# Kernel tuning notes

Hardware: AMD Instinct MI355X
Metric: run time of the kernel (lower is better)

## Reference

```python
import jax, jax.numpy as jnp
import numpy as np

V, H, L, NH, I, P, B, S = 30000, 768, 12, 12, 3072, 512, 8, 512
D = H // NH  # 64, size_per_head
STD = 0.02
LN_EPS = 1e-3  # Keras LayerNormalization default epsilon


def setup_inputs() -> dict:
    key = jax.random.key(0)
    ks = jax.random.split(key, 16)
    n = lambda k, shape: (jax.random.normal(k, shape, jnp.float32) * STD)
    return {
        "input_ids": jax.random.randint(ks[0], (B, S), 0, V, dtype=jnp.int32),
        "input_mask": jnp.ones((B, S), jnp.int32),
        "token_type_ids": jnp.zeros((B, S), jnp.int32),
        "tok_emb": n(ks[1], (V, H)),
        "pos_emb": n(ks[2], (P, H)),
        "type_emb": n(ks[3], (2, H)),
        "emb_ln_g": jnp.ones((H,), jnp.float32),
        "emb_ln_b": jnp.zeros((H,), jnp.float32),
        "Wq": n(ks[4], (L, H, H)), "bq": jnp.zeros((L, H), jnp.float32),
        "Wk": n(ks[5], (L, H, H)), "bk": jnp.zeros((L, H), jnp.float32),
        "Wv": n(ks[6], (L, H, H)), "bv": jnp.zeros((L, H), jnp.float32),
        "Wo": n(ks[7], (L, H, H)), "bo": jnp.zeros((L, H), jnp.float32),
        "ln1_g": jnp.ones((L, H), jnp.float32), "ln1_b": jnp.zeros((L, H), jnp.float32),
        "Wi": n(ks[8], (L, H, I)), "bi": jnp.zeros((L, I), jnp.float32),
        "Wd": n(ks[9], (L, I, H)), "bd": jnp.zeros((L, H), jnp.float32),
        "ln2_g": jnp.ones((L, H), jnp.float32), "ln2_b": jnp.zeros((L, H), jnp.float32),
    }


def layer_norm(x, g, b):
    mu = jnp.mean(x, axis=-1, keepdims=True)
    var = jnp.mean(jnp.square(x - mu), axis=-1, keepdims=True)
    return (x - mu) * jax.lax.rsqrt(var + LN_EPS) * g + b


def bert_forward(input_ids, input_mask, token_type_ids,
                 tok_emb, pos_emb, type_emb, emb_ln_g, emb_ln_b,
                 Wq, bq, Wk, bk, Wv, bv, Wo, bo, ln1_g, ln1_b,
                 Wi, bi, Wd, bd, ln2_g, ln2_b):
    b, s = input_ids.shape
    # embeddings: token + segment + position, then layernorm (dropout off at inference)
    x = tok_emb[input_ids] + type_emb[token_type_ids] + pos_emb[:s][None, :, :]
    x = layer_norm(x, emb_ln_g, emb_ln_b)

    # additive attention bias from 2D mask: (1 - m) * -10000, broadcast over heads/queries
    mask_bias = (1.0 - input_mask.astype(jnp.float32))[:, None, None, :] * -10000.0  # [b,1,1,s]
    scale = 1.0 / np.sqrt(float(D))

    def block(h, p):
        wq, bq_, wk, bk_, wv, bv_, wo, bo_, g1, b1, wi, bi_, wd, bd_, g2, b2 = p
        # QKV projections, split heads -> [b, nh, s, d]
        split = lambda t: t.reshape(b, s, NH, D).transpose(0, 2, 1, 3)
        q = split(h @ wq + bq_)
        k = split(h @ wk + bk_)
        v = split(h @ wv + bv_)
        scores = jnp.einsum('bhqd,bhkd->bhqk', q, k) * scale + mask_bias
        probs = jax.nn.softmax(scores, axis=-1)
        o = jnp.einsum('bhqk,bhkd->bhqd', probs, v)
        o = o.transpose(0, 2, 1, 3).reshape(b, s, H)
        attn = layer_norm(o @ wo + bo_ + h, g1, b1)
        ffn = jax.nn.gelu(attn @ wi + bi_, approximate=False) @ wd + bd_
        out = layer_norm(ffn + attn, g2, b2)
        return out, None

    params = (Wq, bq, Wk, bk, Wv, bv, Wo, bo, ln1_g, ln1_b, Wi, bi, Wd, bd, ln2_g, ln2_b)
    x, _ = jax.lax.scan(block, x, params)
    return x


def reference(input_ids, input_mask, token_type_ids,
              tok_emb, pos_emb, type_emb, emb_ln_g, emb_ln_b,
              Wq, bq, Wk, bk, Wv, bv, Wo, bo, ln1_g, ln1_b,
              Wi, bi, Wd, bd, ln2_g, ln2_b):
    return bert_forward(input_ids, input_mask, token_type_ids,
                        tok_emb, pos_emb, type_emb, emb_ln_g, emb_ln_b,
                        Wq, bq, Wk, bk, Wv, bv, Wo, bo, ln1_g, ln1_b,
                        Wi, bi, Wd, bd, ln2_g, ln2_b)
```

## Files before the change

### kernel.cpp

```cpp
#include <hip/hip_runtime.h>
#include <math.h>

#define NHEADS 12
#define DHEAD  64
#define SEQL   512
#define HID    768
#define IMID   3072
#define NTOK   4096
#define NLAY   12
#define QKVW   2304

typedef __attribute__((ext_vector_type(8))) short short8;
typedef __attribute__((ext_vector_type(4))) float f32x4;

__device__ __forceinline__ short f2b(float f) {
    union { float f; unsigned u; } v; v.f = f;
    unsigned r = (v.u + 0x7fffu + ((v.u >> 16) & 1u)) >> 16;
    return (short)r;
}
__device__ __forceinline__ float b2f(short h) {
    union { unsigned u; float f; } v; v.u = ((unsigned)(unsigned short)h) << 16;
    return v.f;
}
__device__ __forceinline__ void mfma16(f32x4& c, short8 a, short8 b) {
    asm volatile("v_mfma_f32_16x16x32_bf16 %0, %1, %2, %0" : "+v"(c) : "v"(a), "v"(b));
}
__device__ __forceinline__ void accfence() {
    __builtin_amdgcn_sched_barrier(0);
    asm volatile("s_nop 7\ns_nop 7\ns_nop 7\ns_nop 7");
    __builtin_amdgcn_sched_barrier(0);
}
__device__ __forceinline__ void gload_lds16(const void* g, void* l) {
    __builtin_amdgcn_global_load_lds(
        (const __attribute__((address_space(1))) unsigned int*)g,
        (__attribute__((address_space(3))) unsigned int*)l, 16, 0, 0);
}
__device__ __forceinline__ float gelu_f(float v) {
    float x = v * 0.70710678118f;
    float ax = fabsf(x);
    float t = 1.0f / (1.0f + 0.3275911f * ax);
    float p = ((((1.061405429f * t - 1.453152027f) * t) + 1.421413741f) * t
               - 0.284496736f) * t + 0.254829592f;
    float e = p * t * __expf(-x * x);
    float er = 1.0f - e;
    er = x < 0.f ? -er : er;
    return 0.5f * v * (1.0f + er);
}

__global__ __launch_bounds__(256) void wconv_k(
    const float* __restrict__ src, short* __restrict__ dst,
    int K, int N, size_t dlsz, int rowStart, float scale)
{
    __shared__ short t[64][72];
    src += (size_t)blockIdx.z * K * N;
    dst += (size_t)blockIdx.z * dlsz;
    const int k0 = blockIdx.x * 64, n0 = blockIdx.y * 64;
    const int kr = threadIdx.x >> 2, q = threadIdx.x & 3;
    const float* s = src + (size_t)(k0 + kr) * N + n0 + q * 16;
#pragma unroll
    for (int j = 0; j < 16; j += 4) {
        float4 v = *reinterpret_cast<const float4*>(s + j);
        t[q * 16 + j + 0][kr] = f2b(v.x * scale);
        t[q * 16 + j + 1][kr] = f2b(v.y * scale);
        t[q * 16 + j + 2][kr] = f2b(v.z * scale);
        t[q * 16 + j + 3][kr] = f2b(v.w * scale);
    }
    __syncthreads();
    const int r = threadIdx.x >> 2;
    short* d = dst + (size_t)(rowStart + n0 + r) * K + k0 + q * 16;
    *reinterpret_cast<short8*>(d)     = *reinterpret_cast<short8*>(&t[r][q * 16]);
    *reinterpret_cast<short8*>(d + 8) = *reinterpret_cast<short8*>(&t[r][q * 16 + 8]);
}

__global__ __launch_bounds__(256) void bpack_k(
    const float* __restrict__ bq, const float* __restrict__ bk,
    const float* __restrict__ bv, float* __restrict__ dst)
{
    int i = blockIdx.x * 256 + threadIdx.x;
    if (i >= NLAY * QKVW) return;
    int l = i / QKVW, c = i % QKVW;
    float v = c < 768 ? 0.125f * bq[l * 768 + c]
            : c < 1536 ? bk[l * 768 + c - 768] : bv[l * 768 + c - 1536];
    dst[i] = v;
}

__global__ __launch_bounds__(256) void embed_ln_k(
    const int* __restrict__ ids, const int* __restrict__ tti,
    const float* __restrict__ tokE, const float* __restrict__ posE,
    const float* __restrict__ typE, const float* __restrict__ g,
    const float* __restrict__ bb, float* __restrict__ x, short* __restrict__ xb)
{
    __shared__ float red[8];
    const int t = blockIdx.x, s = t & (SEQL - 1);
    const int id = ids[t], ty = tti[t];
    float v[3], sum = 0.f, sq = 0.f;
#pragma unroll
    for (int i = 0; i < 3; ++i) {
        const int c = threadIdx.x + 256 * i;
        float e = tokE[(size_t)id * HID + c] + typE[(size_t)ty * HID + c]
                + posE[(size_t)s * HID + c];
        v[i] = e; sum += e; sq += e * e;
    }
#pragma unroll
    for (int d = 1; d < 64; d <<= 1) { sum += __shfl_xor(sum, d); sq += __shfl_xor(sq, d); }
    const int lane = threadIdx.x & 63, w = threadIdx.x >> 6;
    if (lane == 0) { red[w] = sum; red[4 + w] = sq; }
    __syncthreads();
    sum = red[0] + red[1] + red[2] + red[3];
    sq  = red[4] + red[5] + red[6] + red[7];
    const float mu = sum * (1.0f / 768.0f);
    const float var = sq * (1.0f / 768.0f) - mu * mu;
    const float rstd = rsqrtf(var + 1e-3f);
#pragma unroll
    for (int i = 0; i < 3; ++i) {
        const int c = threadIdx.x + 256 * i;
        float yv = (v[i] - mu) * rstd * g[c] + bb[c];
        x[(size_t)t * HID + c] = yv;
        xb[(size_t)t * HID + c] = f2b(yv);
    }
}

__global__ __launch_bounds__(256) void add_ln_k(
    const float* __restrict__ y, const float* __restrict__ res,
    const float* __restrict__ g, const float* __restrict__ bb,
    float* __restrict__ xout, short* __restrict__ bout, float* __restrict__ fout)
{
    __shared__ float red[8];
    const int t = blockIdx.x;
    float v[3], sum = 0.f, sq = 0.f;
#pragma unroll
    for (int i = 0; i < 3; ++i) {
        const int c = threadIdx.x + 256 * i;
        float e = y[(size_t)t * HID + c] + res[(size_t)t * HID + c];
        v[i] = e; sum += e; sq += e * e;
    }
#pragma unroll
    for (int d = 1; d < 64; d <<= 1) { sum += __shfl_xor(sum, d); sq += __shfl_xor(sq, d); }
    const int lane = threadIdx.x & 63, w = threadIdx.x >> 6;
    if (lane == 0) { red[w] = sum; red[4 + w] = sq; }
    __syncthreads();
    sum = red[0] + red[1] + red[2] + red[3];
    sq  = red[4] + red[5] + red[6] + red[7];
    const float mu = sum * (1.0f / 768.0f);
    const float var = sq * (1.0f / 768.0f) - mu * mu;
    const float rstd = rsqrtf(var + 1e-3f);
#pragma unroll
    for (int i = 0; i < 3; ++i) {
        const int c = threadIdx.x + 256 * i;
        float yv = (v[i] - mu) * rstd * g[c] + bb[c];
        xout[(size_t)t * HID + c] = yv;
        bout[(size_t)t * HID + c] = f2b(yv);
        if (fout) fout[(size_t)t * HID + c] = yv;
    }
}

__global__ __launch_bounds__(256) void add_ln_red_k(
    const short* __restrict__ p0, const short* __restrict__ p1,
    const short* __restrict__ res, const float* __restrict__ g,
    const float* __restrict__ bb, short* __restrict__ bout, float* __restrict__ fout)
{
    __shared__ float red[8];
    const int t = blockIdx.x;
    float v[3], sum = 0.f, sq = 0.f;
#pragma unroll
    for (int i = 0; i < 3; ++i) {
        const int c = threadIdx.x + 256 * i;
        const size_t o = (size_t)t * HID + c;
        float e = b2f(p0[o]) + b2f(p1[o]) + b2f(res[o]);
        v[i] = e; sum += e; sq += e * e;
    }
#pragma unroll
    for (int d = 1; d < 64; d <<= 1) { sum += __shfl_xor(sum, d); sq += __shfl_xor(sq, d); }
    const int lane = threadIdx.x & 63, w = threadIdx.x >> 6;
    if (lane == 0) { red[w] = sum; red[4 + w] = sq; }
    __syncthreads();
    sum = red[0] + red[1] + red[2] + red[3];
    sq  = red[4] + red[5] + red[6] + red[7];
    const float mu = sum * (1.0f / 768.0f);
    const float var = sq * (1.0f / 768.0f) - mu * mu;
    const float rstd = rsqrtf(var + 1e-3f);
#pragma unroll
    for (int i = 0; i < 3; ++i) {
        const int c = threadIdx.x + 256 * i;
        float yv = (v[i] - mu) * rstd * g[c] + bb[c];
        bout[(size_t)t * HID + c] = f2b(yv);
        if (fout) fout[(size_t)t * HID + c] = yv;
    }
}

template<int EPI>
__global__ __launch_bounds__(512, 4) void gemm3_k(
    const short* __restrict__ A, const short* __restrict__ Wt,
    const float* __restrict__ bias, void* __restrict__ Out, int K, int N, int kChunk,
    void* __restrict__ Out2)
{
    __shared__ short sA[3][128 * 32];
    __shared__ short sB[3][128 * 32];
    const int tid = threadIdx.x;
    const int lane = tid & 63, wave = tid >> 6;
    const int wm = wave >> 1, wn = wave & 1;
    const int rl = lane & 15, hi = lane >> 4;

    const int nb = gridDim.x, bid = blockIdx.x;
    const int id = (bid & 7) * (nb >> 3) + (bid >> 3);
    const int m0 = (id & 31) * 128, n0 = (id >> 5) * 128;
    const int kBeg = blockIdx.y * kChunk;

    f32x4 acc[2][4];
#pragma unroll
    for (int i = 0; i < 2; ++i)
#pragma unroll
        for (int j = 0; j < 4; ++j)
            acc[i][j] = (f32x4){0.f, 0.f, 0.f, 0.f};

    auto stage = [&](int buf, int k0) {
        const int gb = wave * 64;
        const int gid = gb + lane;
        const int row = gid >> 2, sg = gid & 3;
        const int ksw = (sg ^ ((row >> 1) & 3)) << 3;
        gload_lds16(&A[(size_t)(m0 + row) * K + k0 + ksw], &sA[buf][gb * 8]);
        gload_lds16(&Wt[(size_t)(n0 + row) * K + k0 + ksw], &sB[buf][gb * 8]);
    };

    const int nIter = kChunk >> 5;
    stage(0, kBeg);
    if (nIter > 1) stage(1, kBeg + 32);
    for (int t = 0; t < nIter; ++t) {
        const int cur = t % 3;
        if (t + 2 < nIter) {
            stage((t + 2) % 3, kBeg + (t + 2) * 32);
            __builtin_amdgcn_sched_barrier(0);
            asm volatile("s_waitcnt vmcnt(4)" ::: "memory");
        } else if (t + 1 < nIter) {
            __builtin_amdgcn_sched_barrier(0);
            asm volatile("s_waitcnt vmcnt(2)" ::: "memory");
        } else {
            __builtin_amdgcn_sched_barrier(0);
            asm volatile("s_waitcnt vmcnt(0)" ::: "memory");
        }
        __builtin_amdgcn_s_barrier();
        __builtin_amdgcn_sched_barrier(0);

        short8 af[2], bfr[4];
#pragma unroll
        for (int f = 0; f < 2; ++f) {
            const int ra = wm * 32 + f * 16 + rl;
            af[f] = *reinterpret_cast<const short8*>(&sA[cur][ra * 32 + ((hi ^ ((ra >> 1) & 3)) << 3)]);
        }
#pragma unroll
        for (int j = 0; j < 4; ++j) {
            const int rb = wn * 64 + j * 16 + rl;
            bfr[j] = *reinterpret_cast<const short8*>(&sB[cur][rb * 32 + ((hi ^ ((rb >> 1) & 3)) << 3)]);
        }
#pragma unroll
        for (int i = 0; i < 2; ++i)
#pragma unroll
            for (int j = 0; j < 4; ++j)
                mfma16(acc[i][j], af[i], bfr[j]);

        asm volatile("s_waitcnt lgkmcnt(0)" ::: "memory");
        __builtin_amdgcn_sched_barrier(0);
        __builtin_amdgcn_s_barrier();
    }
    accfence();

    if (EPI == 5 && n0 >= 1536) {
        short* tl = (short*)&sA[0][0];
        const int b = m0 >> 9, s0 = m0 & 511;
        const int vbase = n0 - 1536;
        const int c = tid >> 2, rq = (tid & 3) << 4;
        const int vcol = vbase + c;
        short* dstRow = (short*)Out2 +
            (((size_t)(b * NHEADS + (vcol >> 6)) * DHEAD + (vcol & 63)) << 9) + s0;
#pragma unroll
        for (int pass = 0; pass < 2; ++pass) {
            if ((wm >> 1) == pass) {
#pragma unroll
                for (int j = 0; j < 4; ++j) {
                    const int cc = wn * 64 + j * 16 + rl;
                    const float bv = bias[n0 + cc];
#pragma unroll
                    for (int i = 0; i < 2; ++i)
#pragma unroll
                        for (int e = 0; e < 4; ++e) {
                            const int r = (wm & 1) * 32 + i * 16 + hi * 4 + e;
                            tl[cc * 68 + r] = f2b(acc[i][j][e] + bv);
                        }
                }
            }
            __builtin_amdgcn_s_barrier();
            *reinterpret_cast<short8*>(dstRow + pass * 64 + rq) =
                *reinterpret_cast<short8*>(&tl[c * 68 + rq]);
            *reinterpret_cast<short8*>(dstRow + pass * 64 + rq + 8) =
                *reinterpret_cast<short8*>(&tl[c * 68 + rq + 8]);
            __builtin_amdgcn_s_barrier();
        }
        return;
    }

    short* skDst = nullptr;
    if (EPI == 6)
        skDst = blockIdx.y == 0 ? (short*)Out : (short*)Out2;
#pragma unroll
    for (int j = 0; j < 4; ++j) {
        const int col = n0 + wn * 64 + j * 16 + rl;
        const float bv = (EPI == 6 && blockIdx.y != 0) ? 0.f : bias[col];
#pragma unroll
        for (int i = 0; i < 2; ++i) {
#pragma unroll
            for (int e = 0; e < 4; ++e) {
                const int row = m0 + wm * 32 + i * 16 + hi * 4 + e;
                float v = acc[i][j][e] + bv;
                if (EPI == 0) {
                    ((float*)Out)[(size_t)row * N + col] = v;
                } else if (EPI == 1) {
                    ((short*)Out)[(size_t)row * N + col] = f2b(gelu_f(v));
                } else if (EPI == 6) {
                    skDst[(size_t)row * N + col] = f2b(v);
                } else {
                    ((short*)Out)[(size_t)row * N + col] = f2b(v);
                }
            }
        }
    }
}

template<int EPI>
__global__ __launch_bounds__(256) void gemm_k(
    const short* __restrict__ A, const float* __restrict__ W,
    const float* __restrict__ bias, void* __restrict__ Out, int K, int N)
{
    __shared__ short sA[128 * 40];
    __shared__ short sB[128 * 40];
    const int tid = threadIdx.x;
    const int lane = tid & 63, wave = tid >> 6;
    const int wm = wave >> 1, wn = wave & 1;
    const int m0 = blockIdx.x * 128, n0 = blockIdx.y * 128;
    const int rl = lane & 15, hi = lane >> 4;

    f32x4 acc[4][4];
#pragma unroll
    for (int i = 0; i < 4; ++i)
#pragma unroll
        for (int j = 0; j < 4; ++j)
            acc[i][j] = (f32x4){0.f, 0.f, 0.f, 0.f};

    const int arow = tid >> 2, ac8 = (tid & 3) << 3;
    const int bk0 = tid >> 5, bn4 = (tid & 31) << 2;

    for (int k0 = 0; k0 < K; k0 += 32) {
#pragma unroll
        for (int i = 0; i < 2; ++i) {
            int row = i * 64 + arow;
            short8 v = *reinterpret_cast<const short8*>(&A[(size_t)(m0 + row) * K + k0 + ac8]);
            *reinterpret_cast<short8*>(&sA[row * 40 + ac8]) = v;
        }
#pragma unroll
        for (int p = 0; p < 4; ++p) {
            int kk = p * 8 + bk0;
            float4 w4 = *reinterpret_cast<const float4*>(&W[(size_t)(k0 + kk) * N + n0 + bn4]);
            sB[(bn4 + 0) * 40 + kk] = f2b(w4.x);
            sB[(bn4 + 1) * 40 + kk] = f2b(w4.y);
            sB[(bn4 + 2) * 40 + kk] = f2b(w4.z);
            sB[(bn4 + 3) * 40 + kk] = f2b(w4.w);
        }
        __syncthreads();
        short8 af[4], bfr[4];
#pragma unroll
        for (int f = 0; f < 4; ++f) {
            af[f]  = *reinterpret_cast<const short8*>(&sA[(wm * 64 + f * 16 + rl) * 40 + hi * 8]);
            bfr[f] = *reinterpret_cast<const short8*>(&sB[(wn * 64 + f * 16 + rl) * 40 + hi * 8]);
        }
#pragma unroll
        for (int i = 0; i < 4; ++i)
#pragma unroll
            for (int j = 0; j < 4; ++j)
                mfma16(acc[i][j], af[i], bfr[j]);
        __syncthreads();
    }
    accfence();
#pragma unroll
    for (int j = 0; j < 4; ++j) {
        const int col = n0 + wn * 64 + j * 16 + rl;
        const float bv = bias[col];
#pragma unroll
        for (int i = 0; i < 4; ++i) {
#pragma unroll
            for (int e = 0; e < 4; ++e) {
                const int row = m0 + wm * 64 + i * 16 + hi * 4 + e;
                float v = acc[i][j][e] + bv;
                if (EPI == 0) {
                    ((float*)Out)[(size_t)row * N + col] = v;
                } else if (EPI == 1) {
                    float gl = 0.5f * v * (1.0f + erff(v * 0.70710678118f));
                    ((short*)Out)[(size_t)row * N + col] = f2b(gl);
                } else {
                    const int b = row >> 9, s = row & 511, nh = col >> 6, d = col & 63;
                    if (EPI == 2)
                        ((short*)Out)[(((size_t)(b * NHEADS + nh) * SEQL + s) << 6) + d] = f2b(v * 0.125f);
                    else if (EPI == 3)
                        ((short*)Out)[(((size_t)(b * NHEADS + nh) * SEQL + s) << 6) + d] = f2b(v);
                    else
                        ((short*)Out)[(((size_t)(b * NHEADS + nh) * DHEAD + d) << 9) + s] = f2b(v);
                }
            }
        }
    }
}

__global__ __launch_bounds__(256) void attn_k(
    const short* __restrict__ qkv, const short* __restrict__ vt,
    const int* __restrict__ mask, short* __restrict__ ctx)
{
    __shared__ short sQ[32 * 72];
    __shared__ short sP[32 * 520];
    __shared__ float wreds[128];

    const int orig = blockIdx.x;
    const int blk = (orig & 7) * (gridDim.x >> 3) + (orig >> 3);
    const int qb = blk & 15, bh = blk >> 4;
    const int b = bh / NHEADS, h = bh % NHEADS;
    const int tid = threadIdx.x, lane = tid & 63, wave = tid >> 6;
    const int rl = lane & 15, hi = lane >> 4;
    const short* __restrict__ qh = qkv + (size_t)(b * SEQL) * QKVW + h * 64;
    const short* __restrict__ kh = qh + 768;
    const short* __restrict__ vh = vt + (size_t)bh * DHEAD * SEQL;

    {
        int row = tid >> 3, c8 = (tid & 7) << 3;
        *reinterpret_cast<short8*>(&sQ[row * 72 + c8]) =
            *reinterpret_cast<const short8*>(&qh[(size_t)(qb * 32 + row) * QKVW + c8]);
    }

    float mb[8];
#pragma unroll
    for (int fn = 0; fn < 8; ++fn) {
        int n = wave * 128 + fn * 16 + rl;
        mb[fn] = -10000.0f * (1.0f - (float)mask[b * SEQL + n]);
    }
    __syncthreads();

    f32x4 sacc[2][8];
#pragma unroll
    for (int mf = 0; mf < 2; ++mf)
#pragma unroll
        for (int fn = 0; fn < 8; ++fn)
            sacc[mf][fn] = (f32x4){0.f, 0.f, 0.f, 0.f};
    __builtin_amdgcn_s_setprio(1);
#pragma unroll
    for (int ks = 0; ks < 2; ++ks) {
        short8 a0 = *reinterpret_cast<const short8*>(&sQ[rl * 72 + ks * 32 + hi * 8]);
        short8 a1 = *reinterpret_cast<const short8*>(&sQ[(16 + rl) * 72 + ks * 32 + hi * 8]);
#pragma unroll
        for (int fn = 0; fn < 8; ++fn) {
            int n = wave * 128 + fn * 16 + rl;
            short8 bk = *reinterpret_cast<const short8*>(&kh[(size_t)n * QKVW + ks * 32 + hi * 8]);
            mfma16(sacc[0][fn], a0, bk);
            mfma16(sacc[1][fn], a1, bk);
        }
    }
    __builtin_amdgcn_s_setprio(0);
    accfence();

    float rsum[2][4] = {{0.f, 0.f, 0.f, 0.f}, {0.f, 0.f, 0.f, 0.f}};
#pragma unroll
    for (int mf = 0; mf < 2; ++mf)
#pragma unroll
        for (int fn = 0; fn < 8; ++fn)
#pragma unroll
            for (int e = 0; e < 4; ++e) {
                float p = __expf(sacc[mf][fn][e] + mb[fn]);
                rsum[mf][e] += p;
                sP[(mf * 16 + hi * 4 + e) * 520 + wave * 128 + fn * 16 + rl] = f2b(p);
            }
#pragma unroll
    for (int d = 1; d < 16; d <<= 1)
#pragma unroll
        for (int mf = 0; mf < 2; ++mf)
#pragma unroll
            for (int e = 0; e < 4; ++e)
                rsum[mf][e] += __shfl_xor(rsum[mf][e], d);
    if (rl == 0) {
#pragma unroll
        for (int mf = 0; mf < 2; ++mf)
#pragma unroll
            for (int e = 0; e < 4; ++e)
                wreds[wave * 32 + mf * 16 + hi * 4 + e] = rsum[mf][e];
    }
    __syncthreads();
    float rsf[2][4];
#pragma unroll
    for (int mf = 0; mf < 2; ++mf)
#pragma unroll
        for (int e = 0; e < 4; ++e) {
            const int row = mf * 16 + hi * 4 + e;
            rsf[mf][e] = wreds[row] + wreds[32 + row] + wreds[64 + row] + wreds[96 + row];
        }

    f32x4 oacc[2];
    oacc[0] = (f32x4){0.f, 0.f, 0.f, 0.f};
    oacc[1] = (f32x4){0.f, 0.f, 0.f, 0.f};
    __builtin_amdgcn_s_setprio(1);
#pragma unroll
    for (int ks = 0; ks < 16; ++ks) {
        short8 p0 = *reinterpret_cast<const short8*>(&sP[rl * 520 + ks * 32 + hi * 8]);
        short8 p1 = *reinterpret_cast<const short8*>(&sP[(16 + rl) * 520 + ks * 32 + hi * 8]);
        short8 bv = *reinterpret_cast<const short8*>(&vh[(size_t)(wave * 16 + rl) * SEQL + ks * 32 + hi * 8]);
        mfma16(oacc[0], p0, bv);
        mfma16(oacc[1], p1, bv);
    }
    __builtin_amdgcn_s_setprio(0);
    accfence();
#pragma unroll
    for (int mf = 0; mf < 2; ++mf) {
#pragma unroll
        for (int e = 0; e < 4; ++e) {
            const int row = mf * 16 + hi * 4 + e;
            const int s = qb * 32 + row;
            const int d = wave * 16 + rl;
            float o = oacc[mf][e] * __builtin_amdgcn_rcpf(rsf[mf][e]);
            ctx[((size_t)(b * SEQL + s)) * HID + h * DHEAD + d] = f2b(o);
        }
    }
}

extern "C" void kernel_launch(void* const* d_in, const int* in_sizes, int n_in,
                              void* d_out, int out_size, void* d_ws, size_t ws_size,
                              hipStream_t stream)
{
    const int*   ids  = (const int*)d_in[0];
    const int*   msk  = (const int*)d_in[1];
    const int*   tti  = (const int*)d_in[2];
    const float* tokE = (const float*)d_in[3];
    const float* posE = (const float*)d_in[4];
    const float* typE = (const float*)d_in[5];
    const float* elg  = (const float*)d_in[6];
    const float* elb  = (const float*)d_in[7];
    const float* Wq   = (const float*)d_in[8];  const float* bq = (const float*)d_in[9];
    const float* Wk   = (const float*)d_in[10]; const float* bk = (const float*)d_in[11];
    const float* Wv   = (const float*)d_in[12]; const float* bv = (const float*)d_in[13];
    const float* Wo   = (const float*)d_in[14]; const float* bo = (const float*)d_in[15];
    const float* g1   = (const float*)d_in[16]; const float* b1 = (const float*)d_in[17];
    const float* Wi   = (const float*)d_in[18]; const float* bi = (const float*)d_in[19];
    const float* Wd   = (const float*)d_in[20]; const float* bd = (const float*)d_in[21];
    const float* g2   = (const float*)d_in[22]; const float* b2 = (const float*)d_in[23];

    if (ws_size < 81788928u) return;
    char* ws = (char*)d_ws;
    float* x    = (float*)(ws);
    short* yb   = (short*)(ws + 12582912);
    short* ppb  = (short*)(ws + 18874368);
    short* vt   = (short*)(ws + 18874368);
    short* xb   = (short*)(ws + 25165824);
    short* qkv  = (short*)(ws + 31457280);
    short* ctx  = (short*)(ws + 50331648);
    short* f1   = (short*)(ws + 56623104);
    float* y    = (float*)(ws + 12582912);
    short* qq   = (short*)(ws + 31457280);
    short* kk_  = (short*)(ws + 37748736);
    short* vv   = (short*)(ws + 44040192);

    embed_ln_k<<<NTOK, 256, 0, stream>>>(ids, tti, tokE, posE, typE, elg, elb, x, xb);

    const bool fast = ws_size >= 251768832u;
    if (fast) {
        short* qkvT = (short*)(ws + 81788928);
        short* woT  = (short*)(ws + 124256256);
        short* wiT  = (short*)(ws + 138412032);
        short* wdT  = (short*)(ws + 195035136);
        float* bqkv = (float*)(ws + 251658240);

        wconv_k<<<dim3(12, 12, NLAY), 256, 0, stream>>>(Wq, qkvT, 768, 768, 2304 * 768, 0, 0.125f);
        wconv_k<<<dim3(12, 12, NLAY), 256, 0, stream>>>(Wk, qkvT, 768, 768, 2304 * 768, 768, 1.0f);
        wconv_k<<<dim3(12, 12, NLAY), 256, 0, stream>>>(Wv, qkvT, 768, 768, 2304 * 768, 1536, 1.0f);
        wconv_k<<<dim3(12, 12, NLAY), 256, 0, stream>>>(Wo, woT, 768, 768, 768 * 768, 0, 1.0f);
        wconv_k<<<dim3(12, 48, NLAY), 256, 0, stream>>>(Wi, wiT, 768, 3072, 3072 * 768, 0, 1.0f);
        wconv_k<<<dim3(48, 12, NLAY), 256, 0, stream>>>(Wd, wdT, 3072, 768, 768 * 3072, 0, 1.0f);
        bpack_k<<<108, 256, 0, stream>>>(bq, bk, bv, bqkv);

        for (int l = 0; l < NLAY; ++l) {
            const size_t oH = (size_t)l * HID, oI = (size_t)l * IMID;
            gemm3_k<5><<<dim3(576, 1), 512, 0, stream>>>(xb, qkvT + (size_t)l * 2304 * 768,
                                                         bqkv + (size_t)l * 2304, qkv, 768, 2304, 768,
                                                         vt);
            attn_k<<<1536, 256, 0, stream>>>(qkv, vt, msk, ctx);
            gemm3_k<6><<<dim3(192, 2), 512, 0, stream>>>(ctx, woT + (size_t)l * 768 * 768,
                                                         bo + oH, yb, 768, 768, 384, ppb);
            add_ln_red_k<<<NTOK, 256, 0, stream>>>(yb, ppb, xb, g1 + oH, b1 + oH, xb, nullptr);
            gemm3_k<1><<<dim3(768, 1), 512, 0, stream>>>(xb, wiT + (size_t)l * 3072 * 768,
                                                         bi + oI, f1, 768, 3072, 768,
                                                         nullptr);
            gemm3_k<6><<<dim3(192, 2), 512, 0, stream>>>(f1, wdT + (size_t)l * 768 * 3072,
                                                         bd + oH, yb, 3072, 768, 1536, ppb);
            add_ln_red_k<<<NTOK, 256, 0, stream>>>(yb, ppb, xb, g2 + oH, b2 + oH, xb,
                                                   (l == NLAY - 1) ? (float*)d_out : nullptr);
        }
    } else {
        const dim3 g6(32, 6), g24(32, 24);
        for (int l = 0; l < NLAY; ++l) {
            const size_t oHH = (size_t)l * HID * HID, oH = (size_t)l * HID;
            const size_t oHI = (size_t)l * HID * IMID, oI = (size_t)l * IMID;
            gemm_k<2><<<g6, 256, 0, stream>>>(xb, Wq + oHH, bq + oH, qq, HID, HID);
            gemm_k<3><<<g6, 256, 0, stream>>>(xb, Wk + oHH, bk + oH, kk_, HID, HID);
            gemm_k<4><<<g6, 256, 0, stream>>>(xb, Wv + oHH, bv + oH, vv, HID, HID);
            attn_k<<<1536, 256, 0, stream>>>(qq, vv, msk, ctx);
            gemm_k<0><<<g6, 256, 0, stream>>>(ctx, Wo + oHH, bo + oH, y, HID, HID);
            add_ln_k<<<NTOK, 256, 0, stream>>>(y, x, g1 + oH, b1 + oH, x, xb, nullptr);
            gemm_k<1><<<g24, 256, 0, stream>>>(xb, Wi + oHI, bi + oI, f1, HID, IMID);
            gemm_k<0><<<g6, 256, 0, stream>>>(f1, Wd + oHI, bd + oH, y, IMID, HID);
            add_ln_k<<<NTOK, 256, 0, stream>>>(y, x, g2 + oH, b2 + oH, x, xb,
                                               (l == NLAY - 1) ? (float*)d_out : nullptr);
        }
    }
}
```

Baseline: 2.043 ms.

## Split FFN down-proj K four ways, widen attention to 8 waves, skip fp32 embed store

The FFN down-projection GEMM now splits K into four chunks (grid y=4) instead of two. Its partials go into buffers reused from ctx/qkv, and a new add_ln_red4_k sums them with the residual. The attention kernel doubles its threads to 512, so each wave handles 64 keys and one 16x16 output tile, giving more waves per block for latency hiding. The embedding LayerNorm also skips the unused fp32 store on the fast path. The changes trade more partial-sum traffic and workspace aliasing for better GPU occupancy on the low-block-count GEMM.

```diff
diff --git a/kernel.cpp b/kernel.cpp
--- a/kernel.cpp
+++ b/kernel.cpp
@@ -115,7 +115,7 @@
     for (int i = 0; i < 3; ++i) {
         const int c = threadIdx.x + 256 * i;
         float yv = (v[i] - mu) * rstd * g[c] + bb[c];
-        x[(size_t)t * HID + c] = yv;
+        if (x) x[(size_t)t * HID + c] = yv;
         xb[(size_t)t * HID + c] = f2b(yv);
     }
 }
@@ -188,11 +188,46 @@
     }
 }
 
+__global__ __launch_bounds__(256) void add_ln_red4_k(
+    const short* __restrict__ p0, const short* __restrict__ p1,
+    const short* __restrict__ p2, const short* __restrict__ p3,
+    const short* __restrict__ res, const float* __restrict__ g,
+    const float* __restrict__ bb, short* __restrict__ bout, float* __restrict__ fout)
+{
+    __shared__ float red[8];
+    const int t = blockIdx.x;
+    float v[3], sum = 0.f, sq = 0.f;
+#pragma unroll
+    for (int i = 0; i < 3; ++i) {
+        const int c = threadIdx.x + 256 * i;
+        const size_t o = (size_t)t * HID + c;
+        float e = (b2f(p0[o]) + b2f(p1[o])) + (b2f(p2[o]) + b2f(p3[o])) + b2f(res[o]);
+        v[i] = e; sum += e; sq += e * e;
+    }
+#pragma unroll
+    for (int d = 1; d < 64; d <<= 1) { sum += __shfl_xor(sum, d); sq += __shfl_xor(sq, d); }
+    const int lane = threadIdx.x & 63, w = threadIdx.x >> 6;
+    if (lane == 0) { red[w] = sum; red[4 + w] = sq; }
+    __syncthreads();
+    sum = red[0] + red[1] + red[2] + red[3];
+    sq  = red[4] + red[5] + red[6] + red[7];
+    const float mu = sum * (1.0f / 768.0f);
+    const float var = sq * (1.0f / 768.0f) - mu * mu;
+    const float rstd = rsqrtf(var + 1e-3f);
+#pragma unroll
+    for (int i = 0; i < 3; ++i) {
+        const int c = threadIdx.x + 256 * i;
+        float yv = (v[i] - mu) * rstd * g[c] + bb[c];
+        bout[(size_t)t * HID + c] = f2b(yv);
+        if (fout) fout[(size_t)t * HID + c] = yv;
+    }
+}
+
 template<int EPI>
 __global__ __launch_bounds__(512, 4) void gemm3_k(
     const short* __restrict__ A, const short* __restrict__ Wt,
     const float* __restrict__ bias, void* __restrict__ Out, int K, int N, int kChunk,
-    void* __restrict__ Out2)
+    void* __restrict__ Out2, void* __restrict__ Out3, void* __restrict__ Out4)
 {
     __shared__ short sA[3][128 * 32];
     __shared__ short sB[3][128 * 32];
@@ -300,7 +335,9 @@
 
     short* skDst = nullptr;
     if (EPI == 6)
-        skDst = blockIdx.y == 0 ? (short*)Out : (short*)Out2;
+        skDst = blockIdx.y == 0 ? (short*)Out
+              : blockIdx.y == 1 ? (short*)Out2
+              : blockIdx.y == 2 ? (short*)Out3 : (short*)Out4;
 #pragma unroll
     for (int j = 0; j < 4; ++j) {
         const int col = n0 + wn * 64 + j * 16 + rl;
@@ -408,13 +445,13 @@
     }
 }
 
-__global__ __launch_bounds__(256) void attn_k(
+__global__ __launch_bounds__(512) void attn_k(
     const short* __restrict__ qkv, const short* __restrict__ vt,
     const int* __restrict__ mask, short* __restrict__ ctx)
 {
     __shared__ short sQ[32 * 72];
     __shared__ short sP[32 * 520];
-    __shared__ float wreds[128];
+    __shared__ float wreds[256];
 
     const int orig = blockIdx.x;
     const int blk = (orig & 7) * (gridDim.x >> 3) + (orig >> 3);
@@ -426,25 +463,25 @@
     const short* __restrict__ kh = qh + 768;
     const short* __restrict__ vh = vt + (size_t)bh * DHEAD * SEQL;
 
-    {
+    if (tid < 256) {
         int row = tid >> 3, c8 = (tid & 7) << 3;
         *reinterpret_cast<short8*>(&sQ[row * 72 + c8]) =
             *reinterpret_cast<const short8*>(&qh[(size_t)(qb * 32 + row) * QKVW + c8]);
     }
 
-    float mb[8];
-#pragma unroll
-    for (int fn = 0; fn < 8; ++fn) {
-        int n = wave * 128 + fn * 16 + rl;
+    float mb[4];
+#pragma unroll
+    for (int fn = 0; fn < 4; ++fn) {
+        int n = wave * 64 + fn * 16 + rl;
         mb[fn] = -10000.0f * (1.0f - (float)mask[b * SEQL + n]);
     }
     __syncthreads();
 
-    f32x4 sacc[2][8];
+    f32x4 sacc[2][4];
 #pragma unroll
     for (int mf = 0; mf < 2; ++mf)
 #pragma unroll
-        for (int fn = 0; fn < 8; ++fn)
+        for (int fn = 0; fn < 4; ++fn)
             sacc[mf][fn] = (f32x4){0.f, 0.f, 0.f, 0.f};
     __builtin_amdgcn_s_setprio(1);
 #pragma unroll
@@ -452,8 +489,8 @@
         short8 a0 = *reinterpret_cast<const short8*>(&sQ[rl * 72 + ks * 32 + hi * 8]);
         short8 a1 = *reinterpret_cast<const short8*>(&sQ[(16 + rl) * 72 + ks * 32 + hi * 8]);
 #pragma unroll
-        for (int fn = 0; fn < 8; ++fn) {
-            int n = wave * 128 + fn * 16 + rl;
+        for (int fn = 0; fn < 4; ++fn) {
+            int n = wave * 64 + fn * 16 + rl;
             short8 bk = *reinterpret_cast<const short8*>(&kh[(size_t)n * QKVW + ks * 32 + hi * 8]);
             mfma16(sacc[0][fn], a0, bk);
             mfma16(sacc[1][fn], a1, bk);
@@ -466,12 +503,12 @@
 #pragma unroll
     for (int mf = 0; mf < 2; ++mf)
 #pragma unroll
-        for (int fn = 0; fn < 8; ++fn)
+        for (int fn = 0; fn < 4; ++fn)
 #pragma unroll
             for (int e = 0; e < 4; ++e) {
                 float p = __expf(sacc[mf][fn][e] + mb[fn]);
                 rsum[mf][e] += p;
-                sP[(mf * 16 + hi * 4 + e) * 520 + wave * 128 + fn * 16 + rl] = f2b(p);
+                sP[(mf * 16 + hi * 4 + e) * 520 + wave * 64 + fn * 16 + rl] = f2b(p);
             }
 #pragma unroll
     for (int d = 1; d < 16; d <<= 1)
@@ -494,33 +531,31 @@
 #pragma unroll
         for (int e = 0; e < 4; ++e) {
             const int row = mf * 16 + hi * 4 + e;
-            rsf[mf][e] = wreds[row] + wreds[32 + row] + wreds[64 + row] + wreds[96 + row];
-        }
-
-    f32x4 oacc[2];
-    oacc[0] = (f32x4){0.f, 0.f, 0.f, 0.f};
-    oacc[1] = (f32x4){0.f, 0.f, 0.f, 0.f};
+            float s0 = wreds[row]       + wreds[32 + row];
+            float s1 = wreds[64 + row]  + wreds[96 + row];
+            float s2 = wreds[128 + row] + wreds[160 + row];
+            float s3 = wreds[192 + row] + wreds[224 + row];
+            rsf[mf][e] = (s0 + s1) + (s2 + s3);
+        }
+
+    const int rh = wave >> 2, db = wave & 3;
+    f32x4 oacc = (f32x4){0.f, 0.f, 0.f, 0.f};
     __builtin_amdgcn_s_setprio(1);
 #pragma unroll
     for (int ks = 0; ks < 16; ++ks) {
-        short8 p0 = *reinterpret_cast<const short8*>(&sP[rl * 520 + ks * 32 + hi * 8]);
-        short8 p1 = *reinterpret_cast<const short8*>(&sP[(16 + rl) * 520 + ks * 32 + hi * 8]);
-        short8 bv = *reinterpret_cast<const short8*>(&vh[(size_t)(wave * 16 + rl) * SEQL + ks * 32 + hi * 8]);
-        mfma16(oacc[0], p0, bv);
-        mfma16(oacc[1], p1, bv);
+        short8 p  = *reinterpret_cast<const short8*>(&sP[(rh * 16 + rl) * 520 + ks * 32 + hi * 8]);
+        short8 bv = *reinterpret_cast<const short8*>(&vh[(size_t)(db * 16 + rl) * SEQL + ks * 32 + hi * 8]);
+        mfma16(oacc, p, bv);
     }
     __builtin_amdgcn_s_setprio(0);
     accfence();
 #pragma unroll
-    for (int mf = 0; mf < 2; ++mf) {
-#pragma unroll
-        for (int e = 0; e < 4; ++e) {
-            const int row = mf * 16 + hi * 4 + e;
-            const int s = qb * 32 + row;
-            const int d = wave * 16 + rl;
-            float o = oacc[mf][e] * __builtin_amdgcn_rcpf(rsf[mf][e]);
-            ctx[((size_t)(b * SEQL + s)) * HID + h * DHEAD + d] = f2b(o);
-        }
+    for (int e = 0; e < 4; ++e) {
+        const int row = rh * 16 + hi * 4 + e;
+        const int s = qb * 32 + row;
+        const int d = db * 16 + rl;
+        float o = oacc[e] * __builtin_amdgcn_rcpf(rsf[rh][e]);
+        ctx[((size_t)(b * SEQL + s)) * HID + h * DHEAD + d] = f2b(o);
     }
 }
 
@@ -555,14 +590,17 @@
     short* qkv  = (short*)(ws + 31457280);
     short* ctx  = (short*)(ws + 50331648);
     short* f1   = (short*)(ws + 56623104);
+    short* pp3  = (short*)(ws + 50331648);
+    short* pp4  = (short*)(ws + 31457280);
     float* y    = (float*)(ws + 12582912);
     short* qq   = (short*)(ws + 31457280);
     short* kk_  = (short*)(ws + 37748736);
     short* vv   = (short*)(ws + 44040192);
 
-    embed_ln_k<<<NTOK, 256, 0, stream>>>(ids, tti, tokE, posE, typE, elg, elb, x, xb);
-
     const bool fast = ws_size >= 251768832u;
+    embed_ln_k<<<NTOK, 256, 0, stream>>>(ids, tti, tokE, posE, typE, elg, elb,
+                                         fast ? nullptr : x, xb);
+
     if (fast) {
         short* qkvT = (short*)(ws + 81788928);
         short* woT  = (short*)(ws + 124256256);
@@ -582,18 +620,20 @@
             const size_t oH = (size_t)l * HID, oI = (size_t)l * IMID;
             gemm3_k<5><<<dim3(576, 1), 512, 0, stream>>>(xb, qkvT + (size_t)l * 2304 * 768,
                                                          bqkv + (size_t)l * 2304, qkv, 768, 2304, 768,
-                                                         vt);
-            attn_k<<<1536, 256, 0, stream>>>(qkv, vt, msk, ctx);
+                                                         vt, nullptr, nullptr);
+            attn_k<<<1536, 512, 0, stream>>>(qkv, vt, msk, ctx);
             gemm3_k<6><<<dim3(192, 2), 512, 0, stream>>>(ctx, woT + (size_t)l * 768 * 768,
-                                                         bo + oH, yb, 768, 768, 384, ppb);
+                                                         bo + oH, yb, 768, 768, 384,
+                                                         ppb, nullptr, nullptr);
             add_ln_red_k<<<NTOK, 256, 0, stream>>>(yb, ppb, xb, g1 + oH, b1 + oH, xb, nullptr);
             gemm3_k<1><<<dim3(768, 1), 512, 0, stream>>>(xb, wiT + (size_t)l * 3072 * 768,
                                                          bi + oI, f1, 768, 3072, 768,
-                                                         nullptr);
-            gemm3_k<6><<<dim3(192, 2), 512, 0, stream>>>(f1, wdT + (size_t)l * 768 * 3072,
-                                                         bd + oH, yb, 3072, 768, 1536, ppb);
-            add_ln_red_k<<<NTOK, 256, 0, stream>>>(yb, ppb, xb, g2 + oH, b2 + oH, xb,
-                                                   (l == NLAY - 1) ? (float*)d_out : nullptr);
+                                                         nullptr, nullptr, nullptr);
+            gemm3_k<6><<<dim3(192, 4), 512, 0, stream>>>(f1, wdT + (size_t)l * 768 * 3072,
+                                                         bd + oH, yb, 3072, 768, 768,
+                                                         ppb, pp3, pp4);
+            add_ln_red4_k<<<NTOK, 256, 0, stream>>>(yb, ppb, pp3, pp4, xb, g2 + oH, b2 + oH, xb,
+                                                    (l == NLAY - 1) ? (float*)d_out : nullptr);
         }
     } else {
         const dim3 g6(32, 6), g24(32, 24);
@@ -603,7 +643,7 @@
             gemm_k<2><<<g6, 256, 0, stream>>>(xb, Wq + oHH, bq + oH, qq, HID, HID);
             gemm_k<3><<<g6, 256, 0, stream>>>(xb, Wk + oHH, bk + oH, kk_, HID, HID);
             gemm_k<4><<<g6, 256, 0, stream>>>(xb, Wv + oHH, bv + oH, vv, HID, HID);
-            attn_k<<<1536, 256, 0, stream>>>(qq, vv, msk, ctx);
+            attn_k<<<1536, 512, 0, stream>>>(qq, vv, msk, ctx);
             gemm_k<0><<<g6, 256, 0, stream>>>(ctx, Wo + oHH, bo + oH, y, HID, HID);
             add_ln_k<<<NTOK, 256, 0, stream>>>(y, x, g1 + oH, b1 + oH, x, xb, nullptr);
             gemm_k<1><<<g24, 256, 0, stream>>>(xb, Wi + oHI, bi + oI, f1, HID, IMID);
```

Result: slower. 2.134 ms (+4.5%).
